# Optimization experiments

Measured on AMD Instinct MI355X. Metric: run time of the kernel, lower is better.

The kernel has to match this reference:

```python
import jax, jax.numpy as jnp
import numpy as np

N_NODES = 100000
N_EDGES = 3200000
IN_CH, HID, OUT_CH = 128, 16, 64


def gcn_conv(x, W, b, row, col, n_nodes):
    # PyG GCNConv: add self loops, symmetric deg^{-1/2} normalization,
    # linear transform, scatter-add aggregation at target nodes (col).
    x = x @ W  # [N, out]
    deg = jax.ops.segment_sum(jnp.ones_like(col, dtype=x.dtype), col,
                              num_segments=n_nodes)  # includes self loops
    inv_sqrt = jnp.where(deg > 0, jax.lax.rsqrt(deg), 0.0)
    norm = inv_sqrt[row] * inv_sqrt[col]  # [E+N]
    msgs = x[row] * norm[:, None]  # gather + scale
    out = jax.ops.segment_sum(msgs, col, num_segments=n_nodes)
    return out + b


def setup_inputs() -> dict:
    key = jax.random.key(0)
    ks = jax.random.split(key, 12)
    x = jax.random.normal(ks[0], (N_NODES, IN_CH), dtype=jnp.float32)
    edge_index = jax.random.randint(ks[1], (2, N_EDGES), 0, N_NODES, dtype=jnp.int64)

    def glorot(k, fan_in, fan_out):
        s = jnp.sqrt(6.0 / (fan_in + fan_out))
        return jax.random.uniform(k, (fan_in, fan_out), jnp.float32, -s, s)

    return {
        'x': x,
        'edge_index': edge_index,
        'conv1_W': glorot(ks[2], IN_CH, HID),
        'conv1_b': jnp.zeros((HID,), jnp.float32),
        'conv2_W': glorot(ks[3], HID, OUT_CH),
        'conv2_b': jnp.zeros((OUT_CH,), jnp.float32),
        't1_W': glorot(ks[4], IN_CH, HID),
        't1_b': jnp.zeros((HID,), jnp.float32),
        't2_W': glorot(ks[5], HID, OUT_CH),
        't2_b': jnp.zeros((OUT_CH,), jnp.float32),
    }


def reference(x, edge_index, conv1_W, conv1_b, conv2_W, conv2_b,
              t1_W, t1_b, t2_W, t2_b):
    n = x.shape[0]
    # add self loops once (fixed shape)
    loops = jnp.arange(n, dtype=edge_index.dtype)
    row = jnp.concatenate([edge_index[0], loops])
    col = jnp.concatenate([edge_index[1], loops])

    identity1 = x @ t1_W + t1_b
    h = jax.nn.relu(gcn_conv(x, conv1_W, conv1_b, row, col, n)) + identity1
    identity2 = h @ t2_W + t2_b
    out = jax.nn.relu(gcn_conv(h, conv2_W, conv2_b, row, col, n)) + identity2
    return out
```

## Files before the change

kernel.cpp:

```cpp
#include <hip/hip_runtime.h>

#define INCH 128
#define C1   16
#define C2   64
#define LOCB 7
#define BNODES (1 << LOCB)
#define CAP  8192
#define ROWBITS 17
#define ROWMASK ((1 << ROWBITS) - 1)
#define SENT 0xFFFFFFFFu
#define ACC2P 9
#define FXS   1024.0f
#define INVFX 0.0009765625f
#define U16B  32768.5f
#define BSH   15
#define BKT_T 1024
#define AGG_T 512

typedef int iv4 __attribute__((ext_vector_type(4)));

__global__ __launch_bounds__(BKT_T) void bucket_kernel(
    const int* __restrict__ row, const int* __restrict__ col,
    int* __restrict__ gcur, int* __restrict__ barr,
    int e, int n, int K, int nblocks)
{
    __shared__ int cnt[1024];
    __shared__ int cur[1024];
    __shared__ int sst[1024];
    int tid = threadIdx.x;
    int e4 = e >> 2;
    long b0 = (long)blockIdx.x * e4 / nblocks;
    long b1 = (long)(blockIdx.x + 1) * e4 / nblocks;
    const iv4* c4p = (const iv4*)col;
    const iv4* r4p = (const iv4*)row;
    cnt[tid] = 0;
    __syncthreads();
    for (long i = b0 + tid; i < b1; i += BKT_T) {
        iv4 c4 = c4p[i], r4 = r4p[i];
        #pragma unroll
        for (int k = 0; k < 4; ++k) {
            unsigned c = (unsigned)c4[k], r = (unsigned)r4[k];
            if (c < (unsigned)n && r < (unsigned)n)
                atomicAdd(&cnt[c >> LOCB], 1);
        }
    }
    if (blockIdx.x == 0) {
        for (int i = e4 * 4 + tid; i < e; i += BKT_T) {
            unsigned c = (unsigned)col[i], r = (unsigned)row[i];
            if (c < (unsigned)n && r < (unsigned)n)
                atomicAdd(&cnt[c >> LOCB], 1);
        }
    }
    __syncthreads();
    if (tid < K) {
        int c = cnt[tid];
        int rel = c ? atomicAdd(&gcur[tid], (c + 15) & ~15) : 0;
        int start = tid * CAP + rel;
        cur[tid] = start;
        sst[tid] = start;
    }
    __syncthreads();
    for (long i = b0 + tid; i < b1; i += BKT_T) {
        iv4 c4 = c4p[i], r4 = r4p[i];
        #pragma unroll
        for (int k = 0; k < 4; ++k) {
            unsigned c = (unsigned)c4[k], r = (unsigned)r4[k];
            if (c < (unsigned)n && r < (unsigned)n) {
                int b = c >> LOCB;
                int slot = atomicAdd(&cur[b], 1);
                if ((unsigned)slot < (unsigned)((b + 1) * CAP))
                    barr[slot] = (int)(r | ((c & (BNODES - 1)) << ROWBITS));
            }
        }
    }
    if (blockIdx.x == 0) {
        for (int i = e4 * 4 + tid; i < e; i += BKT_T) {
            unsigned c = (unsigned)col[i], r = (unsigned)row[i];
            if (c < (unsigned)n && r < (unsigned)n) {
                int b = c >> LOCB;
                int slot = atomicAdd(&cur[b], 1);
                if ((unsigned)slot < (unsigned)((b + 1) * CAP))
                    barr[slot] = (int)(r | ((c & (BNODES - 1)) << ROWBITS));
            }
        }
    }
    __syncthreads();
    if (tid < K) {
        int c = cnt[tid];
        if (c) {
            int start = sst[tid];
            int end = start + c;
            int re  = start + ((c + 15) & ~15);
            int lim = (tid + 1) * CAP;
            if (end > lim) end = lim;
            if (re  > lim) re  = lim;
            for (int j = end; j < re; ++j) barr[j] = (int)SENT;
        }
    }
}

__global__ __launch_bounds__(AGG_T) void degree_kernel(
    const int* __restrict__ barr, const int* __restrict__ gcur,
    int* __restrict__ deg, int n)
{
    __shared__ int lcnt[BNODES];
    int b = blockIdx.x, tid = threadIdx.x;
    if (tid < BNODES) lcnt[tid] = 0;
    __syncthreads();
    int len = gcur[b];
    if (len < 0) len = 0;
    if (len > CAP) len = CAP;
    int len4 = len >> 2;
    const iv4* b4 = (const iv4*)(barr + b * CAP);
    for (int i = tid; i < len4; i += AGG_T) {
        iv4 p4 = b4[i];
        #pragma unroll
        for (int k = 0; k < 4; ++k) {
            unsigned pk = (unsigned)p4[k];
            if ((pk & ROWMASK) < (unsigned)n)
                atomicAdd(&lcnt[(pk >> ROWBITS) & (BNODES - 1)], 1);
        }
    }
    __syncthreads();
    if (tid < BNODES) {
        int node = (b << LOCB) + tid;
        if (node < n) deg[node] = lcnt[tid];
    }
}

__device__ __forceinline__ unsigned short enc16(float v) {
    float c = fminf(fmaxf(v, -31.0f), 31.0f);
    return (unsigned short)(c * FXS + U16B);
}

__global__ __launch_bounds__(256) void linear1_kernel(
    const float* __restrict__ x, const float* __restrict__ W1,
    const float* __restrict__ T1, const float* __restrict__ t1b,
    const int* __restrict__ deg,
    unsigned short* __restrict__ xu16, float* __restrict__ xT1, int n)
{
    __shared__ float WcT[32][INCH + 4];
    __shared__ float xs[16][INCH + 4];
    int tid = threadIdx.x;

    for (int i = tid; i < INCH * C1; i += 256) {
        int k = i >> 4, c = i & 15;
        WcT[c][k]      = W1[i];
        WcT[c + 16][k] = T1[i];
    }
    int node0 = blockIdx.x * 16;
    for (int i = tid; i < 16 * (INCH / 4); i += 256) {
        int r = i >> 5, cc = i & 31;
        int node = node0 + r;
        float4 v = make_float4(0.f, 0.f, 0.f, 0.f);
        if (node < n) v = ((const float4*)x)[(size_t)node * (INCH / 4) + cc];
        ((float4*)&xs[r][0])[cc] = v;
    }
    __syncthreads();

    int ch = tid & 15, nl = tid >> 4;
    int node = node0 + nl;
    if (node >= n) return;
    const float4* xp  = (const float4*)&xs[nl][0];
    const float4* w1p = (const float4*)&WcT[ch][0];
    const float4* w2p = (const float4*)&WcT[ch + 16][0];
    float4 s1 = make_float4(0.f, 0.f, 0.f, 0.f);
    float4 s2 = make_float4(0.f, 0.f, 0.f, 0.f);
    #pragma unroll
    for (int k4 = 0; k4 < INCH / 4; ++k4) {
        float4 xv = xp[k4];
        float4 wa = w1p[k4];
        float4 wb = w2p[k4];
        s1.x += xv.x * wa.x; s1.y += xv.y * wa.y;
        s1.z += xv.z * wa.z; s1.w += xv.w * wa.w;
        s2.x += xv.x * wb.x; s2.y += xv.y * wb.y;
        s2.z += xv.z * wb.z; s2.w += xv.w * wb.w;
    }
    float a1 = (s1.x + s1.y) + (s1.z + s1.w);
    float a2 = (s2.x + s2.y) + (s2.z + s2.w);
    float ic = rsqrtf((float)(deg[node] + 1));
    xu16[(node << 4) + ch] = enc16(a1 * ic);
    xT1[(node << 4) + ch]  = a2 + t1b[ch];
}

#define EDGE_GS(PK, G)                                                        \
    do {                                                                      \
        if (((PK) & ROWMASK) < un) {                                          \
            unsigned long long* _a = &acc[(((PK) >> ROWBITS) & (BNODES - 1))][tb]; \
            _Pragma("unroll")                                                 \
            for (int _j = 0; _j < 4; ++_j) {                                  \
                unsigned _d = (unsigned)(G)[_j];                              \
                atomicAdd(&_a[_j],                                            \
                    ((unsigned long long)(_d >> 16) << 32) | (_d & 0xFFFFu)); \
            }                                                                 \
        }                                                                     \
    } while (0)

#define GATHER_SCATTER(TBL)                                                   \
    {                                                                         \
        int jj = tid >> 1;                                                    \
        for (int i0 = jj * 4; i0 + 3 < len; i0 += (AGG_T * 2)) {              \
            iv4 w = *(const iv4*)(bp + i0);                                   \
            unsigned s0 = (unsigned)w[0] & ROWMASK, s1 = (unsigned)w[1] & ROWMASK; \
            unsigned s2 = (unsigned)w[2] & ROWMASK, s3 = (unsigned)w[3] & ROWMASK; \
            unsigned c0 = s0 < un ? s0 : 0u, c1 = s1 < un ? s1 : 0u;          \
            unsigned c2 = s2 < un ? s2 : 0u, c3 = s3 < un ? s3 : 0u;          \
            iv4 g0 = *(const iv4*)(TBL + ((size_t)c0 << 3) + tb4);            \
            iv4 g1 = *(const iv4*)(TBL + ((size_t)c1 << 3) + tb4);            \
            iv4 g2 = *(const iv4*)(TBL + ((size_t)c2 << 3) + tb4);            \
            iv4 g3 = *(const iv4*)(TBL + ((size_t)c3 << 3) + tb4);            \
            EDGE_GS((unsigned)w[0], g0);                                      \
            EDGE_GS((unsigned)w[1], g1);                                      \
            EDGE_GS((unsigned)w[2], g2);                                      \
            EDGE_GS((unsigned)w[3], g3);                                      \
        }                                                                     \
    }

__global__ __launch_bounds__(AGG_T) void agg1_bucket_kernel(
    const int* __restrict__ barr, const int* __restrict__ gcur,
    const int* __restrict__ deg, const unsigned short* __restrict__ xu16,
    const float* __restrict__ xT1, const float* __restrict__ b1,
    float* __restrict__ h, unsigned short* __restrict__ hu16, int n)
{
    __shared__ unsigned long long acc[BNODES][ACC2P];
    int b = blockIdx.x, tid = threadIdx.x;
    for (int i = tid; i < BNODES * ACC2P; i += AGG_T) (&acc[0][0])[i] = 0ull;
    __syncthreads();

    int len = gcur[b];
    if (len < 0) len = 0;
    if (len > CAP) len = CAP;
    const int* bp = barr + b * CAP;
    const unsigned* tblw = (const unsigned*)xu16;
    unsigned un = (unsigned)n;
    int tb4 = (tid & 1) << 2;
    int tb  = (tid & 1) << 2;

    GATHER_SCATTER(tblw)
    __syncthreads();

    const unsigned* au = (const unsigned*)&acc[0][0];
    for (int t = tid; t < BNODES * C1; t += AGG_T) {
        int loc = t >> 4, ch = t & 15;
        int node = (b << LOCB) + loc;
        if (node >= n) continue;
        int idx = (node << 4) + ch;
        int dg = deg[node];
        unsigned wd = au[loc * (2 * ACC2P) + ch];
        int tot = (int)(wd + xu16[idx] - ((unsigned)(dg + 1) << BSH));
        float ic = rsqrtf((float)(dg + 1));
        float v = (float)tot * INVFX * ic + b1[ch];
        float hv = fmaxf(v, 0.f) + xT1[idx];
        h[idx]    = hv;
        hu16[idx] = enc16(hv * ic);
    }
}

__global__ __launch_bounds__(AGG_T) void agg2_bucket_kernel(
    const int* __restrict__ barr, const int* __restrict__ gcur,
    const int* __restrict__ deg, const unsigned short* __restrict__ hu16,
    const float* __restrict__ h,
    const float* __restrict__ W2, const float* __restrict__ T2,
    const float* __restrict__ b2, const float* __restrict__ t2b,
    float* __restrict__ out, int n)
{
    __shared__ unsigned long long acc[BNODES][ACC2P];
    __shared__ float Wc[C1][128];
    __shared__ float h_s[BNODES][C1];
    __shared__ float accf[BNODES][C1 + 1];
    int b = blockIdx.x, tid = threadIdx.x;
    for (int i = tid; i < BNODES * ACC2P; i += AGG_T) (&acc[0][0])[i] = 0ull;
    for (int i = tid; i < C1 * 128; i += AGG_T) {
        int k = i >> 7, c = i & 127;
        Wc[k][c] = (c < 64) ? W2[k * C2 + c] : T2[k * C2 + (c - 64)];
    }
    {
        int node0 = b << LOCB;
        for (int t = tid; t < BNODES * C1 / 4; t += AGG_T) {
            float4 v = make_float4(0.f, 0.f, 0.f, 0.f);
            if (node0 + (t >> 2) < n) v = ((const float4*)h)[(size_t)node0 * 4 + t];
            ((float4*)&h_s[0][0])[t] = v;
        }
    }
    __syncthreads();

    int len = gcur[b];
    if (len < 0) len = 0;
    if (len > CAP) len = CAP;
    const int* bp = barr + b * CAP;
    const unsigned* tblw = (const unsigned*)hu16;
    unsigned un = (unsigned)n;
    int tb4 = (tid & 1) << 2;
    int tb  = (tid & 1) << 2;

    GATHER_SCATTER(tblw)
    __syncthreads();

    const unsigned* au = (const unsigned*)&acc[0][0];
    for (int t = tid; t < BNODES * C1; t += AGG_T) {
        int loc = t >> 4, ch = t & 15;
        int node = (b << LOCB) + loc;
        float v = 0.f;
        if (node < n) {
            int dg = deg[node];
            unsigned wd = au[loc * (2 * ACC2P) + ch];
            int tot = (int)(wd + hu16[(node << 4) + ch] - ((unsigned)(dg + 1) << BSH));
            v = (float)tot * INVFX * rsqrtf((float)(dg + 1));
        }
        accf[loc][ch] = v;
    }
    __syncthreads();

    int och = tid & 63, g = tid >> 6;
    float w1r[C1], w2r[C1];
    #pragma unroll
    for (int k = 0; k < C1; ++k) { w1r[k] = Wc[k][och]; w2r[k] = Wc[k][och + 64]; }
    float bb = b2[och], tb2 = t2b[och];
    for (int q = 0; q < 16; ++q) {
        int loc = (g << 4) + q;
        int node2 = (b << LOCB) + loc;
        if (node2 >= n) continue;
        float s1 = bb, s2 = tb2;
        #pragma unroll
        for (int k = 0; k < C1; ++k) {
            s1 += accf[loc][k] * w1r[k];
            s2 += h_s[loc][k]  * w2r[k];
        }
        out[(size_t)node2 * C2 + och] = fmaxf(s1, 0.f) + s2;
    }
}

extern "C" void kernel_launch(void* const* d_in, const int* in_sizes, int n_in,
                              void* d_out, int out_size, void* d_ws, size_t ws_size,
                              hipStream_t stream) {
    const float* x   = (const float*)d_in[0];
    const int*   ei  = (const int*)d_in[1];
    const float* W1  = (const float*)d_in[2];
    const float* b1  = (const float*)d_in[3];
    const float* W2  = (const float*)d_in[4];
    const float* b2  = (const float*)d_in[5];
    const float* T1  = (const float*)d_in[6];
    const float* t1b = (const float*)d_in[7];
    const float* T2  = (const float*)d_in[8];
    const float* t2b = (const float*)d_in[9];
    float* out = (float*)d_out;

    const int n = in_sizes[0] / INCH;
    const int e = in_sizes[1] / 2;
    const int* row = ei;
    const int* col = ei + e;
    const int K = (n + BNODES - 1) >> LOCB;

    char* ws = (char*)d_ws;
    int*            gcur = (int*)ws;                  ws += 4096;
    int*            deg  = (int*)ws;                  ws += (size_t)n * 4;
    float*          xT1  = (float*)ws;                ws += (size_t)n * C1 * 4;
    float*          h    = (float*)ws;                ws += (size_t)n * C1 * 4;
    unsigned short* xu16 = (unsigned short*)ws;       ws += (size_t)n * C1 * 2;
    unsigned short* hu16 = (unsigned short*)ws;       ws += (size_t)n * C1 * 2;
    int*            barr = (int*)ws;                  ws += (size_t)K * CAP * 4;

    const int nbb = 390;

    hipMemsetAsync(gcur, 0, 4096, stream);
    bucket_kernel <<<nbb, BKT_T, 0, stream>>>(row, col, gcur, barr, e, n, K, nbb);
    degree_kernel <<<K, AGG_T, 0, stream>>>(barr, gcur, deg, n);

    linear1_kernel <<<(n + 15) / 16, 256, 0, stream>>>(x, W1, T1, t1b, deg, xu16, xT1, n);
    agg1_bucket_kernel<<<K, AGG_T, 0, stream>>>(barr, gcur, deg, xu16, xT1, b1, h, hu16, n);
    agg2_bucket_kernel<<<K, AGG_T, 0, stream>>>(barr, gcur, deg, hu16, h,
                                                W2, T2, b2, t2b, out, n);
}
```

Before: 250.9 us.

## Register-tile linear1 over 4 nodes x 2 channels per thread with 64-node blocks

The first linear layer now processes 64 nodes per 128-thread block. Each thread computes a 4-node by 2-channel tile for both the conv and identity weights, so each weight read from shared memory is reused across several nodes. It also stages x through padded shared rows and writes packed 32-bit u16 pairs and float2 outputs. The aim is to cut shared-memory traffic per FMA and amortise the weight staging over more nodes, at the cost of more registers and fewer, larger blocks.

```diff
diff --git a/kernel.cpp b/kernel.cpp
--- a/kernel.cpp
+++ b/kernel.cpp
@@ -16,6 +16,8 @@
 #define BSH   15
 #define BKT_T 1024
 #define AGG_T 512
+#define XPAD 134
+#define WPAD 132
 
 typedef int iv4 __attribute__((ext_vector_type(4)));
 
@@ -133,54 +135,65 @@
     return (unsigned short)(c * FXS + U16B);
 }
 
-__global__ __launch_bounds__(256) void linear1_kernel(
+__global__ __launch_bounds__(128) void linear1_kernel(
     const float* __restrict__ x, const float* __restrict__ W1,
     const float* __restrict__ T1, const float* __restrict__ t1b,
     const int* __restrict__ deg,
     unsigned short* __restrict__ xu16, float* __restrict__ xT1, int n)
 {
-    __shared__ float WcT[32][INCH + 4];
-    __shared__ float xs[16][INCH + 4];
+    __shared__ float WcT[32][WPAD];
+    __shared__ float xs[64][XPAD];
     int tid = threadIdx.x;
 
-    for (int i = tid; i < INCH * C1; i += 256) {
+    for (int i = tid; i < INCH * C1; i += 128) {
         int k = i >> 4, c = i & 15;
         WcT[c][k]      = W1[i];
         WcT[c + 16][k] = T1[i];
     }
-    int node0 = blockIdx.x * 16;
-    for (int i = tid; i < 16 * (INCH / 4); i += 256) {
-        int r = i >> 5, cc = i & 31;
+    int node0 = blockIdx.x * 64;
+    for (int i = tid; i < 64 * (INCH / 2); i += 128) {
+        int r = i >> 6, cc = i & 63;
         int node = node0 + r;
-        float4 v = make_float4(0.f, 0.f, 0.f, 0.f);
-        if (node < n) v = ((const float4*)x)[(size_t)node * (INCH / 4) + cc];
-        ((float4*)&xs[r][0])[cc] = v;
-    }
-    __syncthreads();
-
-    int ch = tid & 15, nl = tid >> 4;
-    int node = node0 + nl;
-    if (node >= n) return;
-    const float4* xp  = (const float4*)&xs[nl][0];
-    const float4* w1p = (const float4*)&WcT[ch][0];
-    const float4* w2p = (const float4*)&WcT[ch + 16][0];
-    float4 s1 = make_float4(0.f, 0.f, 0.f, 0.f);
-    float4 s2 = make_float4(0.f, 0.f, 0.f, 0.f);
+        float2 v = make_float2(0.f, 0.f);
+        if (node < n) v = ((const float2*)x)[(size_t)node * 64 + cc];
+        *(float2*)&xs[r][cc * 2] = v;
+    }
+    __syncthreads();
+
+    int cg = tid & 7, ng = tid >> 3;
+    int ch0 = cg * 2;
+    const float4* w1a = (const float4*)&WcT[ch0][0];
+    const float4* w1b = (const float4*)&WcT[ch0 + 1][0];
+    const float4* w2a = (const float4*)&WcT[ch0 + 16][0];
+    const float4* w2b = (const float4*)&WcT[ch0 + 17][0];
+    float a1[2][4] = {}, a2[2][4] = {};
+    #pragma unroll 4
+    for (int k4 = 0; k4 < INCH / 4; ++k4) {
+        float4 wa0 = w1a[k4], wa1 = w1b[k4];
+        float4 wb0 = w2a[k4], wb1 = w2b[k4];
+        #pragma unroll
+        for (int j = 0; j < 4; ++j) {
+            int r = ng * 4 + j;
+            float2 xlo = *(const float2*)&xs[r][k4 * 4];
+            float2 xhi = *(const float2*)&xs[r][k4 * 4 + 2];
+            a1[0][j] += xlo.x * wa0.x + xlo.y * wa0.y + xhi.x * wa0.z + xhi.y * wa0.w;
+            a1[1][j] += xlo.x * wa1.x + xlo.y * wa1.y + xhi.x * wa1.z + xhi.y * wa1.w;
+            a2[0][j] += xlo.x * wb0.x + xlo.y * wb0.y + xhi.x * wb0.z + xhi.y * wb0.w;
+            a2[1][j] += xlo.x * wb1.x + xlo.y * wb1.y + xhi.x * wb1.z + xhi.y * wb1.w;
+        }
+    }
+    float tb0 = t1b[ch0], tb1 = t1b[ch0 + 1];
     #pragma unroll
-    for (int k4 = 0; k4 < INCH / 4; ++k4) {
-        float4 xv = xp[k4];
-        float4 wa = w1p[k4];
-        float4 wb = w2p[k4];
-        s1.x += xv.x * wa.x; s1.y += xv.y * wa.y;
-        s1.z += xv.z * wa.z; s1.w += xv.w * wa.w;
-        s2.x += xv.x * wb.x; s2.y += xv.y * wb.y;
-        s2.z += xv.z * wb.z; s2.w += xv.w * wb.w;
-    }
-    float a1 = (s1.x + s1.y) + (s1.z + s1.w);
-    float a2 = (s2.x + s2.y) + (s2.z + s2.w);
-    float ic = rsqrtf((float)(deg[node] + 1));
-    xu16[(node << 4) + ch] = enc16(a1 * ic);
-    xT1[(node << 4) + ch]  = a2 + t1b[ch];
+    for (int j = 0; j < 4; ++j) {
+        int node = node0 + ng * 4 + j;
+        if (node >= n) continue;
+        float ic = rsqrtf((float)(deg[node] + 1));
+        int idx = (node << 4) + ch0;
+        unsigned pk = (unsigned)enc16(a1[0][j] * ic)
+                    | ((unsigned)enc16(a1[1][j] * ic) << 16);
+        *(unsigned*)(xu16 + idx) = pk;
+        *(float2*)(xT1 + idx) = make_float2(a2[0][j] + tb0, a2[1][j] + tb1);
+    }
 }
 
 #define EDGE_GS(PK, G)                                                        \
@@ -366,7 +379,7 @@
     bucket_kernel <<<nbb, BKT_T, 0, stream>>>(row, col, gcur, barr, e, n, K, nbb);
     degree_kernel <<<K, AGG_T, 0, stream>>>(barr, gcur, deg, n);
 
-    linear1_kernel <<<(n + 15) / 16, 256, 0, stream>>>(x, W1, T1, t1b, deg, xu16, xT1, n);
+    linear1_kernel <<<(n + 63) / 64, 128, 0, stream>>>(x, W1, T1, t1b, deg, xu16, xT1, n);
     agg1_bucket_kernel<<<K, AGG_T, 0, stream>>>(barr, gcur, deg, xu16, xT1, b1, h, hu16, n);
     agg2_bucket_kernel<<<K, AGG_T, 0, stream>>>(barr, gcur, deg, hu16, h,
                                                 W2, T2, b2, t2b, out, n);
```

Result: slower. 285.6 us (+13.8%).
